# Kernel tuning notes

Measured on AMD Instinct MI355X. Metric: run time of the kernel, lower is better.

The kernel has to match this reference:

```python
import jax, jax.numpy as jnp
import numpy as np

# loss coefficients (init_kwargs loss_coef_dict)
COEF_CLS = 1.0
COEF_REG = 1.0
COEF_CPT = 0.01


def setup_inputs() -> dict:
    key = jax.random.key(0)
    k1, k2, k3, k4, k5 = jax.random.split(key, 5)
    B, NCLS, K, H, W = 128, 200, 312, 28, 28
    return {
        "class_scores": jax.random.normal(k1, (B, NCLS), dtype=jnp.float32),
        "attr_scores_pred": jax.random.normal(k2, (B, K), dtype=jnp.float32),
        "attr_scores_gt": jax.random.uniform(k3, (B, K), dtype=jnp.float32),
        "attn_maps": jax.random.uniform(k4, (B, K, H, W), dtype=jnp.float32),
        "class_ids": jax.random.randint(k5, (B,), 0, NCLS, dtype=jnp.int64),
    }


def _l_cpt(attn_maps):
    # attn_maps: [b, k, h, w]; per-map argmax location, distance-weighted mean
    b, k, h, w = attn_maps.shape
    maps = attn_maps.reshape(b * k, h, w)
    flat_idx = jnp.argmax(maps.reshape(b * k, h * w), axis=-1)  # [bk]
    ch = (flat_idx // w).astype(attn_maps.dtype)  # row of max
    cw = (flat_idx % w).astype(attn_maps.dtype)   # col of max
    rows = jnp.arange(h, dtype=attn_maps.dtype)[None, :, None]  # grid_h
    cols = jnp.arange(w, dtype=attn_maps.dtype)[None, None, :]  # grid_w
    dist2 = (rows - ch[:, None, None]) ** 2 + (cols - cw[:, None, None]) ** 2
    per_map = jnp.mean(maps * dist2, axis=(1, 2))  # [bk]
    return jnp.mean(per_map)


def reference(class_scores, attr_scores_pred, attr_scores_gt, attn_maps, class_ids):
    # l_cls: mean cross-entropy
    logp = jax.nn.log_softmax(class_scores, axis=-1)
    l_cls = -jnp.mean(jnp.take_along_axis(logp, class_ids[:, None], axis=-1))
    # l_reg: mean squared error
    l_reg = jnp.mean((attr_scores_pred - attr_scores_gt) ** 2)
    # l_cpt: concentration loss
    l_cpt = _l_cpt(attn_maps)
    l_cls = COEF_CLS * l_cls
    l_reg = COEF_REG * l_reg
    l_cpt = COEF_CPT * l_cpt
    l_total = l_cls + l_reg + l_cpt
    return jnp.stack([l_cls, l_reg, l_cpt, l_total])
```

## Files before the change

### kernel.cpp

```cpp
#include <hip/hip_runtime.h>
#include <math.h>

#define BATCH   128
#define NCLS    200
#define KATTR   312
#define MH      28
#define MW      28
#define NMAPS   (BATCH * KATTR)
#define MAP_ELEMS (MH * MW)
#define MAP_GROUPS (MAP_ELEMS / 4)
#define NREG    (BATCH * KATTR)

#define MAPS_PER_WAVE   8
#define WAVES_PER_BLOCK 4
#define MAPS_PER_BLOCK  (MAPS_PER_WAVE * WAVES_PER_BLOCK)
#define CPT_BLOCKS      (NMAPS / MAPS_PER_BLOCK)
#define CLS_BLOCKS      (BATCH / WAVES_PER_BLOCK)
#define REG_BLOCKS      8
#define HEAD_BLOCKS     (CLS_BLOCKS + REG_BLOCKS)
#define TOTAL_BLOCKS    (CPT_BLOCKS + HEAD_BLOCKS)

#define WS_CLS  0
#define WS_REG  (WS_CLS + BATCH)
#define WS_CPT  (WS_REG + REG_BLOCKS)
#define WS_TOTAL (WS_CPT + CPT_BLOCKS)

#define COEF_CLS 1.0f
#define COEF_REG 1.0f
#define COEF_CPT 0.01f

#define ELEM(v4, j) ((j) == 0 ? (v4).x : (j) == 1 ? (v4).y : (j) == 2 ? (v4).z : (v4).w)

typedef float v4f __attribute__((ext_vector_type(4)));

__device__ __forceinline__ float4 ldnt(const float4* p) {
    const v4f r = __builtin_nontemporal_load((const v4f*)p);
    return make_float4(r.x, r.y, r.z, r.w);
}

__global__ __launch_bounds__(256) void apn_main(
    const float* __restrict__ class_scores,
    const float* __restrict__ pred,
    const float* __restrict__ gt,
    const float* __restrict__ attn,
    const int*   __restrict__ class_ids,
    float* __restrict__ ws)
{
    const int tid  = threadIdx.x;
    const int lane = tid & 63;
    const int wave = tid >> 6;
    const int blk  = blockIdx.x;

    __shared__ float lds[WAVES_PER_BLOCK];

    if (blk >= HEAD_BLOCKS) {
        const int cb = blk - HEAD_BLOCKS;
        const int m0 = cb * MAPS_PER_BLOCK + wave * MAPS_PER_WAVE;
        const float4* __restrict__ base =
            (const float4*)(attn + (size_t)m0 * MAP_ELEMS);

        float hfv[4][4], wfv[4][4];
        #pragma unroll
        for (int t = 0; t < 4; ++t) {
            #pragma unroll
            for (int j = 0; j < 4; ++j) {
                const int idx = (lane + 64 * t) * 4 + j;
                const int h = idx / MW;
                hfv[t][j] = (float)h;
                wfv[t][j] = (float)(idx - h * MW);
            }
        }

        const bool tail = (lane < (MAP_GROUPS - 192));
        const float4 z4 = make_float4(0.f, 0.f, 0.f, 0.f);
        const int lane4 = lane << 2;

        float4 cur[4], n1[4], n2[4];

        #pragma unroll
        for (int t = 0; t < 3; ++t) cur[t] = ldnt(base + lane + 64 * t);
        if (tail) cur[3] = ldnt(base + lane + 192); else cur[3] = z4;
        {
            const float4* __restrict__ bp = base + MAP_GROUPS;
            #pragma unroll
            for (int t = 0; t < 3; ++t) n1[t] = ldnt(bp + lane + 64 * t);
            if (tail) n1[3] = ldnt(bp + lane + 192); else n1[3] = z4;
        }

        float wsum = 0.0f;

        #pragma unroll
        for (int mm = 0; mm < MAPS_PER_WAVE; ++mm) {
            if (mm + 2 < MAPS_PER_WAVE) {
                const float4* __restrict__ bp = base + (size_t)(mm + 2) * MAP_GROUPS;
                #pragma unroll
                for (int t = 0; t < 3; ++t) n2[t] = ldnt(bp + lane + 64 * t);
                if (tail) n2[3] = ldnt(bp + lane + 192); else n2[3] = z4;
            }

            float maxv = -INFINITY;
            int   maxi = 0;
            #pragma unroll
            for (int t = 0; t < 4; ++t) {
                #pragma unroll
                for (int j = 0; j < 4; ++j) {
                    const float v = ELEM(cur[t], j);
                    const int idx = lane4 + t * 256 + j;
                    if (v > maxv) { maxv = v; maxi = idx; }
                }
            }

            unsigned long long pk =
                ((unsigned long long)__float_as_uint(maxv) << 32) |
                (unsigned int)(~(unsigned int)maxi);
            #pragma unroll
            for (int off = 1; off < 64; off <<= 1) {
                const unsigned long long o = __shfl_xor(pk, off);
                if (o > pk) pk = o;
            }
            const int bmaxi = (int)(~(unsigned int)pk);

            const float chf = (float)(bmaxi / MW);
            const float cwf = (float)(bmaxi % MW);

            #pragma unroll
            for (int t = 0; t < 4; ++t) {
                #pragma unroll
                for (int j = 0; j < 4; ++j) {
                    const float dh = hfv[t][j] - chf;
                    const float dw = wfv[t][j] - cwf;
                    wsum += ELEM(cur[t], j) * (dh * dh + dw * dw);
                }
            }

            if (mm + 1 < MAPS_PER_WAVE) {
                #pragma unroll
                for (int t = 0; t < 4; ++t) cur[t] = n1[t];
            }
            if (mm + 2 < MAPS_PER_WAVE) {
                #pragma unroll
                for (int t = 0; t < 4; ++t) n1[t] = n2[t];
            }
        }

        #pragma unroll
        for (int off = 1; off < 64; off <<= 1) wsum += __shfl_xor(wsum, off);
        if (lane == 0) lds[wave] = wsum;
        __syncthreads();
        if (tid == 0) ws[WS_CPT + cb] = lds[0] + lds[1] + lds[2] + lds[3];

    } else if (blk < CLS_BLOCKS) {
        const int row = blk * WAVES_PER_BLOCK + wave;
        const float* __restrict__ xr = class_scores + (size_t)row * NCLS;

        float xv[4];
        float m = -INFINITY;
        #pragma unroll
        for (int t = 0; t < 4; ++t) {
            const int c = lane + 64 * t;
            if (c < NCLS) { xv[t] = xr[c]; m = fmaxf(m, xv[t]); }
            else            xv[t] = -INFINITY;
        }
        #pragma unroll
        for (int off = 1; off < 64; off <<= 1) m = fmaxf(m, __shfl_xor(m, off));

        float se = 0.0f;
        #pragma unroll
        for (int t = 0; t < 4; ++t) {
            const int c = lane + 64 * t;
            if (c < NCLS) se += expf(xv[t] - m);
        }
        #pragma unroll
        for (int off = 1; off < 64; off <<= 1) se += __shfl_xor(se, off);

        if (lane == 0) {
            const int cid = class_ids[row];
            const float lse = m + logf(se);
            ws[WS_CLS + row] = lse - xr[cid];
        }

    } else {
        const int rb = blk - CLS_BLOCKS;
        const float4* __restrict__ p = (const float4*)pred;
        const float4* __restrict__ q = (const float4*)gt;
        float s = 0.0f;
        for (int i = rb * 256 + tid; i < NREG / 4; i += REG_BLOCKS * 256) {
            const float4 a = p[i];
            const float4 b = q[i];
            const float dx = a.x - b.x, dy = a.y - b.y, dz = a.z - b.z, dw = a.w - b.w;
            s += dx * dx + dy * dy + dz * dz + dw * dw;
        }
        #pragma unroll
        for (int off = 1; off < 64; off <<= 1) s += __shfl_xor(s, off);
        if (lane == 0) lds[wave] = s;
        __syncthreads();
        if (tid == 0) ws[WS_REG + rb] = lds[0] + lds[1] + lds[2] + lds[3];
    }
}

__global__ __launch_bounds__(256) void apn_final(
    const float* __restrict__ ws, float* __restrict__ out)
{
    const int tid  = threadIdx.x;
    const int lane = tid & 63;
    const int wave = tid >> 6;

    float a = 0.0f, b = 0.0f, c = 0.0f;
    for (int i = tid; i < BATCH; i += 256)      a += ws[WS_CLS + i];
    if (tid < REG_BLOCKS)                       b  = ws[WS_REG + tid];
    for (int i = tid; i < CPT_BLOCKS; i += 256) c += ws[WS_CPT + i];

    #pragma unroll
    for (int off = 1; off < 64; off <<= 1) {
        a += __shfl_xor(a, off);
        b += __shfl_xor(b, off);
        c += __shfl_xor(c, off);
    }

    __shared__ float la[4], lb[4], lc[4];
    if (lane == 0) { la[wave] = a; lb[wave] = b; lc[wave] = c; }
    __syncthreads();
    if (tid == 0) {
        const float sa = la[0] + la[1] + la[2] + la[3];
        const float sb = lb[0] + lb[1] + lb[2] + lb[3];
        const float sc = lc[0] + lc[1] + lc[2] + lc[3];
        const float l_cls = COEF_CLS * (sa / (float)BATCH);
        const float l_reg = COEF_REG * (sb / (float)NREG);
        const float l_cpt = COEF_CPT * (sc / ((float)NMAPS * (float)MAP_ELEMS));
        out[0] = l_cls;
        out[1] = l_reg;
        out[2] = l_cpt;
        out[3] = l_cls + l_reg + l_cpt;
    }
}

extern "C" void kernel_launch(void* const* d_in, const int* in_sizes, int n_in,
                              void* d_out, int out_size, void* d_ws, size_t ws_size,
                              hipStream_t stream) {
    const float* class_scores = (const float*)d_in[0];
    const float* pred         = (const float*)d_in[1];
    const float* gt           = (const float*)d_in[2];
    const float* attn         = (const float*)d_in[3];
    const int*   class_ids    = (const int*)d_in[4];
    float* ws  = (float*)d_ws;
    float* out = (float*)d_out;

    apn_main<<<dim3(TOTAL_BLOCKS), dim3(256), 0, stream>>>(
        class_scores, pred, gt, attn, class_ids, ws);
    apn_final<<<dim3(1), dim3(256), 0, stream>>>(ws, out);
}
```

Before: 183.5 us.

## Cut register use in concentration loop to raise occupancy

Shortens the per-wave prefetch from two maps ahead to one and drops the precomputed row/column coordinate arrays. Coordinates are now recomputed inside the loop with integer division by 28, and launch bounds request 8 blocks per CU. The goal is fewer live VGPRs so more waves can hide memory latency, at the cost of less in-flight load depth per wave and extra integer arithmetic per element.

```diff
diff --git a/kernel.cpp b/kernel.cpp
--- a/kernel.cpp
+++ b/kernel.cpp
@@ -38,7 +38,7 @@
     return make_float4(r.x, r.y, r.z, r.w);
 }
 
-__global__ __launch_bounds__(256) void apn_main(
+__global__ __launch_bounds__(256, 8) void apn_main(
     const float* __restrict__ class_scores,
     const float* __restrict__ pred,
     const float* __restrict__ gt,
@@ -59,43 +59,25 @@
         const float4* __restrict__ base =
             (const float4*)(attn + (size_t)m0 * MAP_ELEMS);
 
-        float hfv[4][4], wfv[4][4];
-        #pragma unroll
-        for (int t = 0; t < 4; ++t) {
-            #pragma unroll
-            for (int j = 0; j < 4; ++j) {
-                const int idx = (lane + 64 * t) * 4 + j;
-                const int h = idx / MW;
-                hfv[t][j] = (float)h;
-                wfv[t][j] = (float)(idx - h * MW);
-            }
-        }
-
         const bool tail = (lane < (MAP_GROUPS - 192));
         const float4 z4 = make_float4(0.f, 0.f, 0.f, 0.f);
         const int lane4 = lane << 2;
 
-        float4 cur[4], n1[4], n2[4];
+        float4 cur[4], n1[4];
 
         #pragma unroll
         for (int t = 0; t < 3; ++t) cur[t] = ldnt(base + lane + 64 * t);
         if (tail) cur[3] = ldnt(base + lane + 192); else cur[3] = z4;
-        {
-            const float4* __restrict__ bp = base + MAP_GROUPS;
-            #pragma unroll
-            for (int t = 0; t < 3; ++t) n1[t] = ldnt(bp + lane + 64 * t);
-            if (tail) n1[3] = ldnt(bp + lane + 192); else n1[3] = z4;
-        }
 
         float wsum = 0.0f;
 
         #pragma unroll
         for (int mm = 0; mm < MAPS_PER_WAVE; ++mm) {
-            if (mm + 2 < MAPS_PER_WAVE) {
-                const float4* __restrict__ bp = base + (size_t)(mm + 2) * MAP_GROUPS;
-                #pragma unroll
-                for (int t = 0; t < 3; ++t) n2[t] = ldnt(bp + lane + 64 * t);
-                if (tail) n2[3] = ldnt(bp + lane + 192); else n2[3] = z4;
+            if (mm + 1 < MAPS_PER_WAVE) {
+                const float4* __restrict__ bp = base + (size_t)(mm + 1) * MAP_GROUPS;
+                #pragma unroll
+                for (int t = 0; t < 3; ++t) n1[t] = ldnt(bp + lane + 64 * t);
+                if (tail) n1[3] = ldnt(bp + lane + 192); else n1[3] = z4;
             }
 
             float maxv = -INFINITY;
@@ -127,8 +109,11 @@
             for (int t = 0; t < 4; ++t) {
                 #pragma unroll
                 for (int j = 0; j < 4; ++j) {
-                    const float dh = hfv[t][j] - chf;
-                    const float dw = wfv[t][j] - cwf;
+                    const int idx = lane4 + t * 256 + j;
+                    const int h = idx / MW;
+                    const int w = idx - h * MW;
+                    const float dh = (float)h - chf;
+                    const float dw = (float)w - cwf;
                     wsum += ELEM(cur[t], j) * (dh * dh + dw * dw);
                 }
             }
@@ -136,10 +121,6 @@
             if (mm + 1 < MAPS_PER_WAVE) {
                 #pragma unroll
                 for (int t = 0; t < 4; ++t) cur[t] = n1[t];
-            }
-            if (mm + 2 < MAPS_PER_WAVE) {
-                #pragma unroll
-                for (int t = 0; t < 4; ++t) n1[t] = n2[t];
             }
         }
 
```

Result: slower. 261.8 us (+42.6%).
